# Kernel tuning notes

Hardware: AMD Instinct MI355X
Metric: run time of the kernel (lower is better)

## Reference

```python
import jax, jax.numpy as jnp
import numpy as np

BETA = 0.9  # leaky-integrator decay of the stateful neuron


def setup_inputs() -> dict:
    key = jax.random.key(0)
    k = jax.random.split(key, 5)
    B, T, I, H, O = 128, 512, 1024, 2048, 512
    x = jax.random.normal(k[0], (B, T, I), dtype=jnp.float32)
    # Linear params, PyTorch-style scaling
    W_in = jax.random.normal(k[1], (I, H), dtype=jnp.float32) / np.sqrt(I)
    b_in = jax.random.normal(k[2], (H,), dtype=jnp.float32) / np.sqrt(I)
    W_out = jax.random.normal(k[3], (H, O), dtype=jnp.float32) / np.sqrt(H)
    b_out = jax.random.normal(k[4], (O,), dtype=jnp.float32) / np.sqrt(H)
    return {"x": x, "W_in": W_in, "b_in": b_in, "W_out": W_out, "b_out": b_out}


def reference(x, W_in, b_in, W_out, b_out):
    # x: [B, T, I]
    B, T, _ = x.shape
    # fc_in applied to every timestep at once (same math as per-step Linear)
    h = jnp.einsum('bti,ih->bth', x, W_in) + b_in  # [B, T, H]

    # stateful neuron: leaky integration s_t = BETA * s_{t-1} + h_t, via scan
    def step(s, h_t):
        s = BETA * s + h_t
        return s, s

    s0 = jnp.zeros((B, h.shape[-1]), dtype=h.dtype)
    _, S = jax.lax.scan(step, s0, jnp.swapaxes(h, 0, 1))  # S: [T, B, H]

    # readout per timestep, then reduce over time (readout_mode='sum')
    logits = jnp.einsum('tbh,ho->tbo', S, W_out) + b_out  # [T, B, O]
    return logits.sum(axis=0)  # [B, O]
```

## Files before the change

### kernel.cpp

```cpp
#include <hip/hip_runtime.h>
#include <hip/hip_bf16.h>
#include <math.h>

constexpr int B_ = 128, T_ = 512, I_ = 1024, H_ = 2048, O_ = 512;
#define BETA 0.9f

constexpr int WOFF = 0;
constexpr int YOFF = 512;
constexpr int ZOFF = YOFF + B_ * I_;
constexpr int WS_FLOATS = ZOFF + B_ * H_;

typedef __attribute__((ext_vector_type(4))) short short4v;
typedef __attribute__((ext_vector_type(4))) float float4v;

__device__ inline void mfma16(float4v& acc, short4v a, short4v b) {
    asm("v_mfma_f32_16x16x16_bf16 %0, %1, %2, %0" : "+v"(acc) : "v"(a), "v"(b));
}

__global__ __launch_bounds__(256) void init_kernel(float* __restrict__ ws,
                                                   const float* __restrict__ b_in,
                                                   const float* __restrict__ b_out,
                                                   float* __restrict__ out, float wsum) {
    int idx = blockIdx.x * 256 + threadIdx.x;
    const int total = WS_FLOATS + B_ * O_;
    if (idx >= total) return;
    if (idx < 512) {
        ws[idx] = (1.0f - powf(BETA, (float)(T_ - idx))) * (1.0f / (1.0f - BETA));
    } else if (idx < ZOFF) {
        ws[idx] = 0.0f;
    } else if (idx < WS_FLOATS) {
        int j = idx - ZOFF;
        ws[idx] = wsum * b_in[j & (H_ - 1)];
    } else {
        int j = idx - WS_FLOATS;
        out[j] = (float)T_ * b_out[j & (O_ - 1)];
    }
}

constexpr int TCH = 32;
__global__ __launch_bounds__(256) void wreduce_kernel(const float* __restrict__ x,
                                                      float* __restrict__ ws) {
    __shared__ float wl[TCH];
    const int b  = blockIdx.x >> 4;
    const int tc = blockIdx.x & 15;
    const int t0 = tc * TCH;
    if (threadIdx.x < TCH) wl[threadIdx.x] = ws[WOFF + t0 + threadIdx.x];
    __syncthreads();

    const int i = threadIdx.x * 4;
    const float* xp = x + (size_t)b * T_ * I_ + (size_t)t0 * I_ + i;
    float4v acc = {0.f, 0.f, 0.f, 0.f};
#pragma unroll
    for (int tb = 0; tb < TCH; tb += 8) {
        float4v v[8];
#pragma unroll
        for (int j = 0; j < 8; ++j)
            v[j] = __builtin_nontemporal_load((const float4v*)(xp + (size_t)(tb + j) * I_));
#pragma unroll
        for (int j = 0; j < 8; ++j) {
            const float wt = wl[tb + j];
            acc.x += wt * v[j].x; acc.y += wt * v[j].y;
            acc.z += wt * v[j].z; acc.w += wt * v[j].w;
        }
    }
    float* yp = ws + YOFF + b * I_ + i;
    atomicAdd(yp + 0, acc.x);
    atomicAdd(yp + 1, acc.y);
    atomicAdd(yp + 2, acc.z);
    atomicAdd(yp + 3, acc.w);
}

template <int KGLOB, int NGLOB, int KCH>
__global__ __launch_bounds__(256) void mm128(const float* __restrict__ A,
                                             const float* __restrict__ Bm,
                                             float* __restrict__ C) {
    constexpr int BN = 64, BK = 32, PAD = 8;
    __shared__ __hip_bfloat16 As[128][BK + PAD];
    __shared__ __hip_bfloat16 Bs[BN][BK + PAD];

    const int n0    = blockIdx.x * BN;
    const int kbase = blockIdx.y * KCH;
    const int tid   = threadIdx.x;
    const int lane  = tid & 63;
    const int w     = tid >> 6;
    const int lo    = lane & 15;
    const int hi    = lane >> 4;

    float4v acc[2][4];
#pragma unroll
    for (int mf = 0; mf < 2; ++mf)
#pragma unroll
        for (int nf = 0; nf < 4; ++nf) acc[mf][nf] = (float4v){0.f, 0.f, 0.f, 0.f};

    for (int k0 = kbase; k0 < kbase + KCH; k0 += BK) {
        {
            const int row = tid >> 1;
            const int kh  = (tid & 1) * 16;
            const float* ap = A + (size_t)row * KGLOB + k0 + kh;
#pragma unroll
            for (int j = 0; j < 4; ++j) {
                float4 v = *(const float4*)(ap + 4 * j);
                union { short4v s; __hip_bfloat16 h[4]; } u;
                u.h[0] = __float2bfloat16(v.x); u.h[1] = __float2bfloat16(v.y);
                u.h[2] = __float2bfloat16(v.z); u.h[3] = __float2bfloat16(v.w);
                *(short4v*)&As[row][kh + 4 * j] = u.s;
            }
        }
        {
            const int k  = tid >> 3;
            const int nq = (tid & 7) * 8;
            const float* bp = Bm + (size_t)(k0 + k) * NGLOB + n0 + nq;
#pragma unroll
            for (int j = 0; j < 2; ++j) {
                float4 v = *(const float4*)(bp + 4 * j);
                Bs[nq + 4 * j + 0][k] = __float2bfloat16(v.x);
                Bs[nq + 4 * j + 1][k] = __float2bfloat16(v.y);
                Bs[nq + 4 * j + 2][k] = __float2bfloat16(v.z);
                Bs[nq + 4 * j + 3][k] = __float2bfloat16(v.w);
            }
        }
        __syncthreads();
#pragma unroll
        for (int ks = 0; ks < 2; ++ks) {
            const int kk = ks * 16 + 4 * hi;
            short4v a[2], bf[4];
#pragma unroll
            for (int mf = 0; mf < 2; ++mf)
                a[mf] = *(const short4v*)&As[w * 32 + mf * 16 + lo][kk];
#pragma unroll
            for (int nf = 0; nf < 4; ++nf)
                bf[nf] = *(const short4v*)&Bs[nf * 16 + lo][kk];
#pragma unroll
            for (int mf = 0; mf < 2; ++mf)
#pragma unroll
                for (int nf = 0; nf < 4; ++nf) mfma16(acc[mf][nf], a[mf], bf[nf]);
        }
        __syncthreads();
    }
#pragma unroll
    for (int mf = 0; mf < 2; ++mf)
#pragma unroll
        for (int nf = 0; nf < 4; ++nf)
#pragma unroll
            for (int i = 0; i < 4; ++i) {
                const int row = w * 32 + mf * 16 + hi * 4 + i;
                const int col = n0 + nf * 16 + lo;
                atomicAdd(&C[(size_t)row * NGLOB + col], acc[mf][nf][i]);
            }
}

extern "C" void kernel_launch(void* const* d_in, const int* in_sizes, int n_in,
                              void* d_out, int out_size, void* d_ws, size_t ws_size,
                              hipStream_t stream) {
    const float* x     = (const float*)d_in[0];
    const float* W_in  = (const float*)d_in[1];
    const float* b_in  = (const float*)d_in[2];
    const float* W_out = (const float*)d_in[3];
    const float* b_out = (const float*)d_in[4];
    float* out = (float*)d_out;
    float* ws  = (float*)d_ws;

    const double beta = 0.9;
    const double bT = pow(beta, (double)T_);
    const float wsum = (float)(((double)T_ - beta * (1.0 - bT) / (1.0 - beta)) / (1.0 - beta));

    const int total = WS_FLOATS + B_ * O_;
    init_kernel<<<(total + 255) / 256, 256, 0, stream>>>(ws, b_in, b_out, out, wsum);

    wreduce_kernel<<<B_ * (T_ / TCH), 256, 0, stream>>>(x, ws);

    mm128<I_, H_, 256><<<dim3(H_ / 64, I_ / 256), 256, 0, stream>>>(ws + YOFF, W_in, ws + ZOFF);

    mm128<H_, O_, 256><<<dim3(O_ / 64, H_ / 256), 256, 0, stream>>>(ws + ZOFF, W_out, out);
}
```

Measured before the change: 86.06 us.

## Precompute W_in·W_out product and fuse it with x time-reduction in one launch

Measured after the change: 131.9 us. 53.3% more time.

```diff
diff --git a/kernel.cpp b/kernel.cpp
--- a/kernel.cpp
+++ b/kernel.cpp
@@ -1,90 +1,160 @@
 #include <hip/hip_runtime.h>
-#include <hip/hip_bf16.h>
 #include <math.h>
 
 constexpr int B_ = 128, T_ = 512, I_ = 1024, H_ = 2048, O_ = 512;
-#define BETA 0.9f
-
-constexpr int WOFF = 0;
-constexpr int YOFF = 512;
-constexpr int ZOFF = YOFF + B_ * I_;
-constexpr int WS_FLOATS = ZOFF + B_ * H_;
 
 typedef __attribute__((ext_vector_type(4))) short short4v;
+typedef __attribute__((ext_vector_type(8))) short short8v;
 typedef __attribute__((ext_vector_type(4))) float float4v;
+
+__device__ inline ushort f2bf(float f) {
+    union { float f; unsigned u; } c; c.f = f;
+    return (ushort)((c.u + 0x7FFF + ((c.u >> 16) & 1)) >> 16);
+}
 
 __device__ inline void mfma16(float4v& acc, short4v a, short4v b) {
     asm("v_mfma_f32_16x16x16_bf16 %0, %1, %2, %0" : "+v"(acc) : "v"(a), "v"(b));
 }
 
-__global__ __launch_bounds__(256) void init_kernel(float* __restrict__ ws,
-                                                   const float* __restrict__ b_in,
-                                                   const float* __restrict__ b_out,
-                                                   float* __restrict__ out, float wsum) {
-    int idx = blockIdx.x * 256 + threadIdx.x;
-    const int total = WS_FLOATS + B_ * O_;
-    if (idx >= total) return;
-    if (idx < 512) {
-        ws[idx] = (1.0f - powf(BETA, (float)(T_ - idx))) * (1.0f / (1.0f - BETA));
-    } else if (idx < ZOFF) {
-        ws[idx] = 0.0f;
-    } else if (idx < WS_FLOATS) {
-        int j = idx - ZOFF;
-        ws[idx] = wsum * b_in[j & (H_ - 1)];
+__global__ __launch_bounds__(256) void zero_y(float* __restrict__ ws) {
+    const int i = (blockIdx.x * 256 + threadIdx.x) * 4;
+    *(float4v*)(ws + i) = (float4v){0.f, 0.f, 0.f, 0.f};
+}
+
+__global__ __launch_bounds__(256) void fusedA(const float* __restrict__ x,
+                                              const float* __restrict__ W_in,
+                                              const float* __restrict__ b_in,
+                                              const float* __restrict__ W_out,
+                                              const float* __restrict__ b_out,
+                                              float* __restrict__ ws,
+                                              float* __restrict__ out, float wsum) {
+    __shared__ __align__(16) char smraw[(128 * 40 + 64 * 40) * 2];
+    const int bid = blockIdx.x, tid = threadIdx.x;
+
+    if (bid < 64) {
+        ushort* As = (ushort*)smraw;
+        ushort* Bs = As + 128 * 40;
+        ushort* wc = (ushort*)(ws + B_ * I_);
+        const int m0 = (bid >> 3) * 128, n0 = (bid & 7) * 64;
+        const int lane = tid & 63, w = tid >> 6, lo = lane & 15, hi = lane >> 4;
+
+        float4v acc[2][4];
+#pragma unroll
+        for (int mf = 0; mf < 2; ++mf)
+#pragma unroll
+            for (int nf = 0; nf < 4; ++nf) acc[mf][nf] = (float4v){0.f, 0.f, 0.f, 0.f};
+
+        for (int k0 = 0; k0 < H_; k0 += 32) {
+            {
+                const int row = tid >> 1, kh = (tid & 1) * 16;
+                const float* ap = W_in + (size_t)(m0 + row) * H_ + k0 + kh;
+#pragma unroll
+                for (int j = 0; j < 4; ++j) {
+                    float4v v = *(const float4v*)(ap + 4 * j);
+                    short4v s;
+                    s[0] = (short)f2bf(v.x); s[1] = (short)f2bf(v.y);
+                    s[2] = (short)f2bf(v.z); s[3] = (short)f2bf(v.w);
+                    *(short4v*)&As[row * 40 + kh + 4 * j] = s;
+                }
+            }
+            {
+                const int k = tid >> 3, nq = (tid & 7) * 8;
+                const float* bp = W_out + (size_t)(k0 + k) * O_ + n0 + nq;
+#pragma unroll
+                for (int j = 0; j < 2; ++j) {
+                    float4v v = *(const float4v*)(bp + 4 * j);
+                    Bs[(nq + 4 * j + 0) * 40 + k] = f2bf(v.x);
+                    Bs[(nq + 4 * j + 1) * 40 + k] = f2bf(v.y);
+                    Bs[(nq + 4 * j + 2) * 40 + k] = f2bf(v.z);
+                    Bs[(nq + 4 * j + 3) * 40 + k] = f2bf(v.w);
+                }
+            }
+            __syncthreads();
+#pragma unroll
+            for (int ks = 0; ks < 2; ++ks) {
+                const int kk = ks * 16 + 4 * hi;
+                short4v a[2], bfr[4];
+#pragma unroll
+                for (int mf = 0; mf < 2; ++mf)
+                    a[mf] = *(const short4v*)&As[(w * 32 + mf * 16 + lo) * 40 + kk];
+#pragma unroll
+                for (int nf = 0; nf < 4; ++nf)
+                    bfr[nf] = *(const short4v*)&Bs[(nf * 16 + lo) * 40 + kk];
+#pragma unroll
+                for (int mf = 0; mf < 2; ++mf)
+#pragma unroll
+                    for (int nf = 0; nf < 4; ++nf) mfma16(acc[mf][nf], a[mf], bfr[nf]);
+            }
+            __syncthreads();
+        }
+#pragma unroll
+        for (int mf = 0; mf < 2; ++mf)
+#pragma unroll
+            for (int nf = 0; nf < 4; ++nf)
+#pragma unroll
+                for (int i = 0; i < 4; ++i) {
+                    const int row = w * 32 + mf * 16 + hi * 4 + i;
+                    const int col = n0 + nf * 16 + lo;
+                    wc[(size_t)(m0 + row) * O_ + col] = f2bf(acc[mf][nf][i]);
+                }
+    } else if (bid < 72) {
+        float* red = (float*)smraw;
+        float* bvl = red + 256;
+        const int bb = bid - 64, c0 = bb * 64;
+        const int cl = tid & 63, sl = tid >> 6;
+        const int col = c0 + cl;
+        float s = 0.f;
+        const float* wp = W_out + (size_t)sl * 512 * O_ + col;
+        for (int h = 0; h < 512; ++h) s += b_in[sl * 512 + h] * wp[(size_t)h * O_];
+        red[sl * 64 + cl] = s;
+        __syncthreads();
+        if (tid < 64) {
+            float tot = red[tid] + red[64 + tid] + red[128 + tid] + red[192 + tid];
+            bvl[tid] = (float)T_ * b_out[c0 + tid] + wsum * tot;
+        }
+        __syncthreads();
+        const float val = bvl[cl];
+        for (int r = sl; r < B_; r += 4) out[(size_t)r * O_ + col] = val;
     } else {
-        int j = idx - WS_FLOATS;
-        out[j] = (float)T_ * b_out[j & (O_ - 1)];
+        float* wl = (float*)smraw;
+        const int wb = bid - 72;
+        const int b = wb >> 4, tc = wb & 15, t0 = tc * 32;
+        if (tid < 32)
+            wl[tid] = (1.f - powf(0.9f, (float)(T_ - (t0 + tid)))) * 10.f;
+        __syncthreads();
+        const int i = tid * 4;
+        const float* xp = x + (size_t)b * T_ * I_ + (size_t)t0 * I_ + i;
+        float4v acc = {0.f, 0.f, 0.f, 0.f};
+#pragma unroll
+        for (int tb = 0; tb < 32; tb += 8) {
+            float4v v[8];
+#pragma unroll
+            for (int j = 0; j < 8; ++j)
+                v[j] = __builtin_nontemporal_load((const float4v*)(xp + (size_t)(tb + j) * I_));
+#pragma unroll
+            for (int j = 0; j < 8; ++j) {
+                const float wt = wl[tb + j];
+                acc.x += wt * v[j].x; acc.y += wt * v[j].y;
+                acc.z += wt * v[j].z; acc.w += wt * v[j].w;
+            }
+        }
+        float* yp = ws + b * I_ + i;
+        atomicAdd(yp + 0, acc.x);
+        atomicAdd(yp + 1, acc.y);
+        atomicAdd(yp + 2, acc.z);
+        atomicAdd(yp + 3, acc.w);
     }
 }
 
-constexpr int TCH = 32;
-__global__ __launch_bounds__(256) void wreduce_kernel(const float* __restrict__ x,
-                                                      float* __restrict__ ws) {
-    __shared__ float wl[TCH];
-    const int b  = blockIdx.x >> 4;
-    const int tc = blockIdx.x & 15;
-    const int t0 = tc * TCH;
-    if (threadIdx.x < TCH) wl[threadIdx.x] = ws[WOFF + t0 + threadIdx.x];
-    __syncthreads();
-
-    const int i = threadIdx.x * 4;
-    const float* xp = x + (size_t)b * T_ * I_ + (size_t)t0 * I_ + i;
-    float4v acc = {0.f, 0.f, 0.f, 0.f};
-#pragma unroll
-    for (int tb = 0; tb < TCH; tb += 8) {
-        float4v v[8];
-#pragma unroll
-        for (int j = 0; j < 8; ++j)
-            v[j] = __builtin_nontemporal_load((const float4v*)(xp + (size_t)(tb + j) * I_));
-#pragma unroll
-        for (int j = 0; j < 8; ++j) {
-            const float wt = wl[tb + j];
-            acc.x += wt * v[j].x; acc.y += wt * v[j].y;
-            acc.z += wt * v[j].z; acc.w += wt * v[j].w;
-        }
-    }
-    float* yp = ws + YOFF + b * I_ + i;
-    atomicAdd(yp + 0, acc.x);
-    atomicAdd(yp + 1, acc.y);
-    atomicAdd(yp + 2, acc.z);
-    atomicAdd(yp + 3, acc.w);
-}
-
-template <int KGLOB, int NGLOB, int KCH>
-__global__ __launch_bounds__(256) void mm128(const float* __restrict__ A,
-                                             const float* __restrict__ Bm,
-                                             float* __restrict__ C) {
-    constexpr int BN = 64, BK = 32, PAD = 8;
-    __shared__ __hip_bfloat16 As[128][BK + PAD];
-    __shared__ __hip_bfloat16 Bs[BN][BK + PAD];
-
-    const int n0    = blockIdx.x * BN;
-    const int kbase = blockIdx.y * KCH;
-    const int tid   = threadIdx.x;
-    const int lane  = tid & 63;
-    const int w     = tid >> 6;
-    const int lo    = lane & 15;
-    const int hi    = lane >> 4;
+__global__ __launch_bounds__(256) void finalB(const float* __restrict__ ws,
+                                              float* __restrict__ out) {
+    __shared__ __align__(16) char smraw[(128 * 40 + 64 * 40) * 2];
+    ushort* As = (ushort*)smraw;
+    ushort* Bs = As + 128 * 40;
+    const float* y = ws;
+    const ushort* wc = (const ushort*)(ws + B_ * I_);
+    const int n0 = blockIdx.x * 64, kbase = blockIdx.y * 256;
+    const int tid = threadIdx.x, lane = tid & 63, w = tid >> 6, lo = lane & 15, hi = lane >> 4;
 
     float4v acc[2][4];
 #pragma unroll
@@ -92,48 +162,40 @@
 #pragma unroll
         for (int nf = 0; nf < 4; ++nf) acc[mf][nf] = (float4v){0.f, 0.f, 0.f, 0.f};
 
-    for (int k0 = kbase; k0 < kbase + KCH; k0 += BK) {
+    for (int k0 = kbase; k0 < kbase + 256; k0 += 32) {
         {
-            const int row = tid >> 1;
-            const int kh  = (tid & 1) * 16;
-            const float* ap = A + (size_t)row * KGLOB + k0 + kh;
+            const int row = tid >> 1, kh = (tid & 1) * 16;
+            const float* ap = y + (size_t)row * I_ + k0 + kh;
 #pragma unroll
             for (int j = 0; j < 4; ++j) {
-                float4 v = *(const float4*)(ap + 4 * j);
-                union { short4v s; __hip_bfloat16 h[4]; } u;
-                u.h[0] = __float2bfloat16(v.x); u.h[1] = __float2bfloat16(v.y);
-                u.h[2] = __float2bfloat16(v.z); u.h[3] = __float2bfloat16(v.w);
-                *(short4v*)&As[row][kh + 4 * j] = u.s;
+                float4v v = *(const float4v*)(ap + 4 * j);
+                short4v s;
+                s[0] = (short)f2bf(v.x); s[1] = (short)f2bf(v.y);
+                s[2] = (short)f2bf(v.z); s[3] = (short)f2bf(v.w);
+                *(short4v*)&As[row * 40 + kh + 4 * j] = s;
             }
         }
         {
-            const int k  = tid >> 3;
-            const int nq = (tid & 7) * 8;
-            const float* bp = Bm + (size_t)(k0 + k) * NGLOB + n0 + nq;
-#pragma unroll
-            for (int j = 0; j < 2; ++j) {
-                float4 v = *(const float4*)(bp + 4 * j);
-                Bs[nq + 4 * j + 0][k] = __float2bfloat16(v.x);
-                Bs[nq + 4 * j + 1][k] = __float2bfloat16(v.y);
-                Bs[nq + 4 * j + 2][k] = __float2bfloat16(v.z);
-                Bs[nq + 4 * j + 3][k] = __float2bfloat16(v.w);
-            }
+            const int k = tid >> 3, nq = (tid & 7) * 8;
+            short8v bv = *(const short8v*)&wc[(size_t)(k0 + k) * O_ + n0 + nq];
+#pragma unroll
+            for (int c = 0; c < 8; ++c) Bs[(nq + c) * 40 + k] = (ushort)bv[c];
         }
         __syncthreads();
 #pragma unroll
         for (int ks = 0; ks < 2; ++ks) {
             const int kk = ks * 16 + 4 * hi;
-            short4v a[2], bf[4];
+            short4v a[2], bfr[4];
 #pragma unroll
             for (int mf = 0; mf < 2; ++mf)
-                a[mf] = *(const short4v*)&As[w * 32 + mf * 16 + lo][kk];
+                a[mf] = *(const short4v*)&As[(w * 32 + mf * 16 + lo) * 40 + kk];
 #pragma unroll
             for (int nf = 0; nf < 4; ++nf)
-                bf[nf] = *(const short4v*)&Bs[nf * 16 + lo][kk];
+                bfr[nf] = *(const short4v*)&Bs[(nf * 16 + lo) * 40 + kk];
 #pragma unroll
             for (int mf = 0; mf < 2; ++mf)
 #pragma unroll
-                for (int nf = 0; nf < 4; ++nf) mfma16(acc[mf][nf], a[mf], bf[nf]);
+                for (int nf = 0; nf < 4; ++nf) mfma16(acc[mf][nf], a[mf], bfr[nf]);
         }
         __syncthreads();
     }
@@ -145,7 +207,7 @@
             for (int i = 0; i < 4; ++i) {
                 const int row = w * 32 + mf * 16 + hi * 4 + i;
                 const int col = n0 + nf * 16 + lo;
-                atomicAdd(&C[(size_t)row * NGLOB + col], acc[mf][nf][i]);
+                atomicAdd(&out[(size_t)row * O_ + col], acc[mf][nf][i]);
             }
 }
 
@@ -164,12 +226,7 @@
     const double bT = pow(beta, (double)T_);
     const float wsum = (float)(((double)T_ - beta * (1.0 - bT) / (1.0 - beta)) / (1.0 - beta));
 
-    const int total = WS_FLOATS + B_ * O_;
-    init_kernel<<<(total + 255) / 256, 256, 0, stream>>>(ws, b_in, b_out, out, wsum);
-
-    wreduce_kernel<<<B_ * (T_ / TCH), 256, 0, stream>>>(x, ws);
-
-    mm128<I_, H_, 256><<<dim3(H_ / 64, I_ / 256), 256, 0, stream>>>(ws + YOFF, W_in, ws + ZOFF);
-
-    mm128<H_, O_, 256><<<dim3(O_ / 64, H_ / 256), 256, 0, stream>>>(ws + ZOFF, W_out, out);
-}
+    zero_y<<<B_ * I_ / 1024, 256, 0, stream>>>(ws);
+    fusedA<<<64 + 8 + B_ * (T_ / 32), 256, 0, stream>>>(x, W_in, b_in, W_out, b_out, ws, out, wsum);
+    finalB<<<dim3(O_ / 64, 4), 256, 0, stream>>>(ws, out);
+}
```

## Precompose W_in·W_out into a single weight matrix and fold the bias via b_in·W_out

Applied to the files above, without the earlier changes.

Result: slower. 115.7 us (+34.4%).

```diff
diff --git a/kernel.cpp b/kernel.cpp
--- a/kernel.cpp
+++ b/kernel.cpp
@@ -7,8 +7,8 @@
 
 constexpr int WOFF = 0;
 constexpr int YOFF = 512;
-constexpr int ZOFF = YOFF + B_ * I_;
-constexpr int WS_FLOATS = ZOFF + B_ * H_;
+constexpr int WCOFF = YOFF + B_ * I_;
+constexpr int WS_FLOATS = WCOFF + I_ * O_;
 
 typedef __attribute__((ext_vector_type(4))) short short4v;
 typedef __attribute__((ext_vector_type(4))) float float4v;
@@ -17,24 +17,38 @@
     asm("v_mfma_f32_16x16x16_bf16 %0, %1, %2, %0" : "+v"(acc) : "v"(a), "v"(b));
 }
 
-__global__ __launch_bounds__(256) void init_kernel(float* __restrict__ ws,
-                                                   const float* __restrict__ b_in,
+__global__ __launch_bounds__(256) void init_kernel(float* __restrict__ ws) {
+    int idx = blockIdx.x * 256 + threadIdx.x;
+    if (idx >= WS_FLOATS) return;
+    if (idx < 512) {
+        ws[idx] = (1.0f - powf(BETA, (float)(T_ - idx))) * (1.0f / (1.0f - BETA));
+    } else {
+        ws[idx] = 0.0f;
+    }
+}
+
+__global__ __launch_bounds__(256) void bias_kernel(const float* __restrict__ b_in,
+                                                   const float* __restrict__ W_out,
                                                    const float* __restrict__ b_out,
                                                    float* __restrict__ out, float wsum) {
-    int idx = blockIdx.x * 256 + threadIdx.x;
-    const int total = WS_FLOATS + B_ * O_;
-    if (idx >= total) return;
-    if (idx < 512) {
-        ws[idx] = (1.0f - powf(BETA, (float)(T_ - idx))) * (1.0f / (1.0f - BETA));
-    } else if (idx < ZOFF) {
-        ws[idx] = 0.0f;
-    } else if (idx < WS_FLOATS) {
-        int j = idx - ZOFF;
-        ws[idx] = wsum * b_in[j & (H_ - 1)];
-    } else {
-        int j = idx - WS_FLOATS;
-        out[j] = (float)T_ * b_out[j & (O_ - 1)];
+    __shared__ float red[256];
+    __shared__ float bvl[64];
+    const int c0 = blockIdx.x * 64;
+    const int tid = threadIdx.x;
+    const int cl = tid & 63, sl = tid >> 6;
+    const int col = c0 + cl;
+    float s = 0.f;
+    const float* wp = W_out + (size_t)sl * 512 * O_ + col;
+    for (int h = 0; h < 512; ++h) s += b_in[sl * 512 + h] * wp[(size_t)h * O_];
+    red[sl * 64 + cl] = s;
+    __syncthreads();
+    if (tid < 64) {
+        float tot = red[tid] + red[64 + tid] + red[128 + tid] + red[192 + tid];
+        bvl[tid] = (float)T_ * b_out[c0 + tid] + wsum * tot;
     }
+    __syncthreads();
+    const float val = bvl[cl];
+    for (int r = sl; r < B_; r += 4) out[(size_t)r * O_ + col] = val;
 }
 
 constexpr int TCH = 32;
@@ -80,6 +94,7 @@
 
     const int n0    = blockIdx.x * BN;
     const int kbase = blockIdx.y * KCH;
+    const int m0    = blockIdx.z * 128;
     const int tid   = threadIdx.x;
     const int lane  = tid & 63;
     const int w     = tid >> 6;
@@ -96,7 +111,7 @@
         {
             const int row = tid >> 1;
             const int kh  = (tid & 1) * 16;
-            const float* ap = A + (size_t)row * KGLOB + k0 + kh;
+            const float* ap = A + (size_t)(m0 + row) * KGLOB + k0 + kh;
 #pragma unroll
             for (int j = 0; j < 4; ++j) {
                 float4 v = *(const float4*)(ap + 4 * j);
@@ -143,7 +158,7 @@
         for (int nf = 0; nf < 4; ++nf)
 #pragma unroll
             for (int i = 0; i < 4; ++i) {
-                const int row = w * 32 + mf * 16 + hi * 4 + i;
+                const int row = m0 + w * 32 + mf * 16 + hi * 4 + i;
                 const int col = n0 + nf * 16 + lo;
                 atomicAdd(&C[(size_t)row * NGLOB + col], acc[mf][nf][i]);
             }
@@ -164,12 +179,13 @@
     const double bT = pow(beta, (double)T_);
     const float wsum = (float)(((double)T_ - beta * (1.0 - bT) / (1.0 - beta)) / (1.0 - beta));
 
-    const int total = WS_FLOATS + B_ * O_;
-    init_kernel<<<(total + 255) / 256, 256, 0, stream>>>(ws, b_in, b_out, out, wsum);
+    init_kernel<<<(WS_FLOATS + 255) / 256, 256, 0, stream>>>(ws);
+
+    bias_kernel<<<8, 256, 0, stream>>>(b_in, W_out, b_out, out, wsum);
+
+    mm128<H_, O_, 256><<<dim3(O_ / 64, H_ / 256, I_ / 128), 256, 0, stream>>>(W_in, W_out, ws + WCOFF);
 
     wreduce_kernel<<<B_ * (T_ / TCH), 256, 0, stream>>>(x, ws);
 
-    mm128<I_, H_, 256><<<dim3(H_ / 64, I_ / 256), 256, 0, stream>>>(ws + YOFF, W_in, ws + ZOFF);
-
-    mm128<H_, O_, 256><<<dim3(O_ / 64, H_ / 256), 256, 0, stream>>>(ws + ZOFF, W_out, out);
+    mm128<I_, O_, 256><<<dim3(O_ / 64, I_ / 256, 1), 256, 0, stream>>>(ws + YOFF, ws + WCOFF, out);
 }
```
